# Optimization experiments

Hardware: AMD Instinct MI355X
Metric: run time of the kernel (lower is better)

The kernel has to match this reference:

```python
import jax, jax.numpy as jnp
import numpy as np

H, N, L = 1024, 64, 2          # d_model, d_state, n_layers
B, T, STEPS = 32, 512, 16


def setup_inputs():
    key = jax.random.key(0)
    ks = jax.random.split(key, 12)
    inp = {}
    inp["input_seq"] = jax.random.normal(ks[0], (B, T, 1), jnp.float32)
    inp["autoregressive_steps"] = STEPS
    # input_proj: Linear(1, d_model)
    inp["in_proj_w"] = jax.random.normal(ks[1], (1, H), jnp.float32)
    inp["in_proj_b"] = jnp.zeros((H,), jnp.float32)
    # per-layer diagonal S4 (S4D-style) params, stacked over layers
    inp["log_dt"] = jnp.log(1e-3) + jax.random.uniform(ks[2], (L, H), jnp.float32) * (jnp.log(1e-1) - jnp.log(1e-3))
    inp["A_re"] = -0.5 * jnp.ones((L, H, N), jnp.float32)
    inp["A_im"] = jnp.broadcast_to(jnp.pi * jnp.arange(N, dtype=jnp.float32), (L, H, N)) + jnp.zeros((L, H, N), jnp.float32)
    inp["B_re"] = jax.random.normal(ks[3], (L, H, N), jnp.float32)
    inp["B_im"] = jax.random.normal(ks[4], (L, H, N), jnp.float32)
    inp["C_re"] = jax.random.normal(ks[5], (L, H, N), jnp.float32) / np.sqrt(N)
    inp["C_im"] = jax.random.normal(ks[6], (L, H, N), jnp.float32) / np.sqrt(N)
    inp["D"] = jax.random.normal(ks[7], (L, H), jnp.float32)
    # S4Block output linear with GLU: Linear(H, 2H) then glu
    inp["out_w"] = jax.random.normal(ks[8], (L, H, 2 * H), jnp.float32) / np.sqrt(H)
    inp["out_b"] = jnp.zeros((L, 2 * H), jnp.float32)
    inp["ln_g"] = jnp.ones((L, H), jnp.float32)
    inp["ln_b"] = jnp.zeros((L, H), jnp.float32)
    # output_layer: Linear(d_model, 1)
    inp["head_w"] = jax.random.normal(ks[9], (H, 1), jnp.float32) / np.sqrt(H)
    inp["head_b"] = jnp.zeros((1,), jnp.float32)
    return inp


def _ln(x, g, b, eps=1e-5):
    m = x.mean(-1, keepdims=True)
    v = jnp.var(x, axis=-1, keepdims=True)
    return (x - m) / jnp.sqrt(v + eps) * g + b


def _glu(z):
    a, b = jnp.split(z, 2, axis=-1)
    return a * jax.nn.sigmoid(b)


def _forward(input_seq, in_proj_w, in_proj_b, log_dt, A_re, A_im, B_re, B_im,
             C_re, C_im, D, out_w, out_b, ln_g, ln_b, head_w, head_b, steps):
    Bb = input_seq.shape[0]
    A = A_re + 1j * A_im                              # (L,H,N) complex64
    dt = jnp.exp(log_dt)[..., None]                   # (L,H,1)
    dA = jnp.exp(dt * A)                              # ZOH discretization
    dB = (dA - 1.0) / A * (B_re + 1j * B_im)
    C = C_re + 1j * C_im

    def s4_seq(u, j):  # u: (B,T,H) -> (B,T,H), recurrence over the full sequence
        s0 = jnp.zeros((Bb, H, N), dA.dtype)
        def step(s, ut):  # ut: (B,H)
            s = dA[j] * s + dB[j] * ut[..., None]
            y = 2.0 * jnp.einsum('hn,bhn->bh', C[j], s).real + D[j] * ut
            return s, y
        _, ys = jax.lax.scan(step, s0, jnp.swapaxes(u, 0, 1))
        return jnp.swapaxes(ys, 0, 1)

    # ---- encoder pass over the input sequence ----
    x = input_seq @ in_proj_w + in_proj_b             # (B,T,H)
    for j in range(L):
        res = x
        y = s4_seq(x, j)
        y = jax.nn.gelu(y, approximate=False)
        y = _glu(y @ out_w[j] + out_b[j])
        x = _ln(y + res, ln_g[j], ln_b[j])
    context = x[:, -1, :]                             # (B,H)

    def dec_step(carry, i):
        dec_in, states = carry                        # (B,), (L,B,H,N) complex
        u0 = jnp.broadcast_to(dec_in[:, None], (Bb, H))   # scalar broadcast to d_model
        dec = u0
        new_states = []
        for j in range(L):
            s = dA[j] * states[j] + dB[j] * dec[..., None]
            y = 2.0 * jnp.einsum('hn,bhn->bh', C[j], s).real + D[j] * dec
            y = jax.nn.gelu(y, approximate=False)
            y = _glu(y @ out_w[j] + out_b[j])
            res = jnp.where(i == 0, u0, y)            # step 0: raw-input residual; else self-residual
            dec = _ln(y + res, ln_g[j], ln_b[j])
            new_states.append(s)
        dec = dec + context
        bit = jax.nn.sigmoid(dec @ head_w + head_b)   # (B,1)
        return (bit[:, 0], jnp.stack(new_states)), bit

    s_init = jnp.zeros((L, Bb, H, N), dA.dtype)
    d_init = jnp.zeros((Bb,), input_seq.dtype)
    _, outs = jax.lax.scan(dec_step, (d_init, s_init), jnp.arange(steps))
    return jnp.swapaxes(outs, 0, 1)                   # (B, steps, 1)


def reference(input_seq, in_proj_w, in_proj_b, log_dt, A_re, A_im, B_re, B_im,
              C_re, C_im, D, out_w, out_b, ln_g, ln_b, head_w, head_b,
              autoregressive_steps):
    return _forward(input_seq, in_proj_w, in_proj_b, log_dt, A_re, A_im, B_re,
                    B_im, C_re, C_im, D, out_w, out_b, ln_g, ln_b, head_w,
                    head_b, autoregressive_steps)
```

## Files before the change

### kernel.cpp

```cpp
#include <hip/hip_runtime.h>
#include <hip/hip_bf16.h>
#include <math.h>

#define H    1024
#define NST  64
#define LAYN 2
#define BSZ  32
#define TLEN 512
#define NSTEPS 16
#define H2   2048
#define FLAGSTRIDE 32
#define NGRP 8

typedef __attribute__((ext_vector_type(8))) short bf16x8;
typedef __attribute__((ext_vector_type(4))) float f32x4;

__device__ __forceinline__ float gelu_f(float x){
    return 0.5f*x*(1.0f+erff(x*0.7071067811865475f));
}
__device__ __forceinline__ float sigm_f(float x){
    return 1.0f/(1.0f+expf(-x));
}
__device__ __forceinline__ short bfbits(float x){
    __hip_bfloat16 h = __float2bfloat16(x);
    return *(short*)&h;
}
__device__ __forceinline__ float bf2f(short s){
    unsigned int u = ((unsigned int)(unsigned short)s) << 16;
    return __uint_as_float(u);
}
__device__ __forceinline__ void gload16(const void* g, void* l){
    __builtin_amdgcn_global_load_lds((const __attribute__((address_space(1))) void*)g,
                                     (__attribute__((address_space(3))) void*)l, 16, 0, 0);
}
__device__ __forceinline__ void ast(float* p, float v){
    __hip_atomic_store(p, v, __ATOMIC_RELAXED, __HIP_MEMORY_SCOPE_AGENT);
}
__device__ __forceinline__ float ald(const float* p){
    return __hip_atomic_load(p, __ATOMIC_RELAXED, __HIP_MEMORY_SCOPE_AGENT);
}

__global__ void k_precompute(const float* __restrict__ log_dt,
                             const float* __restrict__ Are, const float* __restrict__ Aim,
                             const float* __restrict__ Bre, const float* __restrict__ Bim,
                             float* __restrict__ dAr, float* __restrict__ dAi,
                             float* __restrict__ dBr, float* __restrict__ dBi){
    int i = blockIdx.x*256 + threadIdx.x;
    if (i >= LAYN*H*NST) return;
    int lh = i / NST;
    float dt = expf(log_dt[lh]);
    float ar = Are[i], ai = Aim[i];
    float e  = expf(dt*ar);
    float sa, ca; sincosf(dt*ai, &sa, &ca);
    float dar = e*ca, dai = e*sa;
    float zr = dar-1.0f, zi = dai;
    float inv = 1.0f/(ar*ar + ai*ai);
    float wr = (zr*ar + zi*ai)*inv;
    float wi = (zi*ar - zr*ai)*inv;
    float br = Bre[i], bi = Bim[i];
    dAr[i]=dar; dAi[i]=dai;
    dBr[i]=wr*br - wi*bi;
    dBi[i]=wr*bi + wi*br;
}

__global__ void k_inproj_x(const float* __restrict__ in, const float* __restrict__ w,
                           const float* __restrict__ bias, float* __restrict__ x){
    int i = blockIdx.x*256+threadIdx.x;
    int h = i & (H-1);
    int bt = i >> 10;
    x[i] = in[bt]*w[h] + bias[h];
}
__global__ void k_inproj_xT(const float* __restrict__ in, const float* __restrict__ w,
                            const float* __restrict__ bias, float* __restrict__ xT){
    int i = blockIdx.x*256+threadIdx.x;
    int t = i & (TLEN-1);
    int bh = i >> 9;
    int h = bh & (H-1);
    int b = bh >> 10;
    xT[i] = in[b*TLEN + t]*w[h] + bias[h];
}

__global__ __launch_bounds__(64) void k_genK(
        const float* __restrict__ dAr, const float* __restrict__ dAi,
        const float* __restrict__ dBr, const float* __restrict__ dBi,
        const float* __restrict__ Cre, const float* __restrict__ Cim,
        float* __restrict__ Kbuf){
    __shared__ float trans[16][65];
    int lh = blockIdx.x;
    int lane = threadIdx.x;
    int pi = lh*NST + lane;
    float ar=dAr[pi], ai=dAi[pi];
    float br=dBr[pi], bi=dBi[pi];
    float cr=2.f*Cre[pi], ci=2.f*Cim[pi];
    float wr = cr*br - ci*bi;
    float wi = cr*bi + ci*br;
    float* Krow = Kbuf + (size_t)lh*TLEN;
    int r = lane>>2, q = lane&3;
    for (int c=0;c<TLEN/16;c++){
        #pragma unroll
        for (int i=0;i<16;i++){
            trans[i][lane] = wr;
            float nr = fmaf(wr,ar, -wi*ai);
            float ni = fmaf(wr,ai,  wi*ar);
            wr=nr; wi=ni;
        }
        __syncthreads();
        float s = 0.f;
        #pragma unroll
        for (int m=0;m<16;m++) s += trans[r][q*16+m];
        s += __shfl_xor(s,1,64);
        s += __shfl_xor(s,2,64);
        if (q==0) Krow[c*16 + r] = s;
        __syncthreads();
    }
}

__global__ __launch_bounds__(256, 2) void k_conv_mfma(
        const float* __restrict__ u,
        const float* __restrict__ Kbuf,
        const float* __restrict__ Dv,
        __hip_bfloat16* __restrict__ g,
        int layer){
    __shared__ short Krp[8][1040];
    __shared__ short u_s[32][520];
    int h = blockIdx.x;
    int tid = threadIdx.x;
    const float* Krow = Kbuf + ((size_t)layer*H + h)*TLEN;
    for (int idx = tid; idx < 8*1040; idx += 256){
        int c = idx / 1040, y = idx - c*1040;
        int x = y + c;
        float v = (x <= 511) ? Krow[511 - x] : 0.f;
        Krp[c][y] = bfbits(v);
    }
    for (int idx = tid; idx < 32*512; idx += 256){
        int b = idx >> 9, t = idx & 511;
        u_s[b][t] = bfbits(u[((size_t)b*H + h)*TLEN + t]);
    }
    __syncthreads();
    int w = tid >> 6, lane = tid & 63;
    int m = lane & 15, q = lane >> 4;
    f32x4 acc[8][2] = {};
    for (int jt = 0; jt < 16; ++jt){
        int jtile = jt*32;
        bf16x8 b0 = *(const bf16x8*)&u_s[m][jtile + q*8];
        bf16x8 b1 = *(const bf16x8*)&u_s[16 + m][jtile + q*8];
        int mi_min = (2*jt - w + 3) >> 2;
        if (mi_min < 0) mi_min = 0;
        #pragma unroll
        for (int mi = 0; mi < 8; ++mi){
            if (mi < mi_min) continue;
            int tb = (mi*4 + w)*16 + m;
            int x0 = 511 - tb + jtile + q*8;
            int c = x0 & 7, base = x0 - c;
            bf16x8 a = *(const bf16x8*)&Krp[c][base];
            acc[mi][0] = __builtin_amdgcn_mfma_f32_16x16x32_bf16(a, b0, acc[mi][0], 0,0,0);
            acc[mi][1] = __builtin_amdgcn_mfma_f32_16x16x32_bf16(a, b1, acc[mi][1], 0,0,0);
        }
    }
    float dv = Dv[layer*H + h];
    #pragma unroll
    for (int mi = 0; mi < 8; ++mi){
        int tb2 = (mi*4 + w)*16 + (lane>>4)*4;
        #pragma unroll
        for (int nf = 0; nf < 2; ++nf){
            int b = nf*16 + (lane & 15);
            short4 o;
            float uu0 = bf2f(u_s[b][tb2+0]);
            float uu1 = bf2f(u_s[b][tb2+1]);
            float uu2 = bf2f(u_s[b][tb2+2]);
            float uu3 = bf2f(u_s[b][tb2+3]);
            o.x = bfbits(gelu_f(fmaf(dv, uu0, acc[mi][nf][0])));
            o.y = bfbits(gelu_f(fmaf(dv, uu1, acc[mi][nf][1])));
            o.z = bfbits(gelu_f(fmaf(dv, uu2, acc[mi][nf][2])));
            o.w = bfbits(gelu_f(fmaf(dv, uu3, acc[mi][nf][3])));
            *(short4*)((short*)g + ((size_t)b*H + h)*TLEN + tb2) = o;
        }
    }
}

__global__ __launch_bounds__(256) void k_trcast_bf(const __hip_bfloat16* __restrict__ x,
                                                   __hip_bfloat16* __restrict__ y){
    __shared__ __hip_bfloat16 tile[32][34];
    int t0 = blockIdx.x*32, h0 = blockIdx.y*32, b = blockIdx.z;
    int tx = threadIdx.x & 31, ty = threadIdx.x >> 5;
    #pragma unroll
    for (int i=0;i<32;i+=8)
        tile[ty+i][tx] = x[((size_t)(b*H + h0+ty+i))*TLEN + t0+tx];
    __syncthreads();
    #pragma unroll
    for (int i=0;i<32;i+=8)
        y[((size_t)(b*TLEN + t0+ty+i))*H + h0+tx] = tile[tx][ty+i];
}

__global__ __launch_bounds__(256) void k_transpose(const float* __restrict__ x, float* __restrict__ xT){
    __shared__ float tile[32][33];
    int t0 = blockIdx.x*32, h0 = blockIdx.y*32, b = blockIdx.z;
    int tx = threadIdx.x & 31, ty = threadIdx.x >> 5;
    #pragma unroll
    for (int i=0;i<32;i+=8)
        tile[ty+i][tx] = x[((size_t)(b*TLEN + t0+ty+i))*H + h0+tx];
    __syncthreads();
    #pragma unroll
    for (int i=0;i<32;i+=8)
        xT[((size_t)(b*H + h0+ty+i))*TLEN + t0+tx] = tile[tx][ty+i];
}

__global__ __launch_bounds__(256) void k_wtr(const float* __restrict__ W,
                                             __hip_bfloat16* __restrict__ Wt){
    __shared__ float tile[32][33];
    int n0 = blockIdx.x*32, k0 = blockIdx.y*32, l = blockIdx.z;
    const float* Wl = W + (size_t)l*H*H2;
    __hip_bfloat16* Wtl = Wt + (size_t)l*H*H2;
    int tx = threadIdx.x & 31, ty = threadIdx.x >> 5;
    #pragma unroll
    for (int i=0;i<32;i+=8)
        tile[ty+i][tx] = Wl[(size_t)(k0+ty+i)*H2 + n0+tx];
    __syncthreads();
    #pragma unroll
    for (int i=0;i<32;i+=8)
        Wtl[(size_t)(n0+ty+i)*H + k0+tx] = __float2bfloat16(tile[tx][ty+i]);
}

__global__ __launch_bounds__(256) void k_gemm_glu_mfma(
        const __hip_bfloat16* __restrict__ Abf,
        const __hip_bfloat16* __restrict__ Wt,
        const float* __restrict__ bias2,
        float* __restrict__ glu){
    __shared__ alignas(16) short As[128*32];
    __shared__ alignas(16) short Bs[128*32];
    const int K = 1024;
    int tid = threadIdx.x;
    int lane = tid & 63, wid = tid >> 6;
    int m0 = blockIdx.x * 128;
    int nb = blockIdx.y * 64;
    int g0 = tid, g1 = tid + 256;
    int r0 = g0 >> 2, r1 = g1 >> 2;
    int wtr0 = nb + ((r0>>6)<<5) + (r0&31) + ((r0>>5)&1)*1024;
    int wtr1 = nb + ((r1>>6)<<5) + (r1&31) + ((r1>>5)&1)*1024;
    const short* Ap = (const short*)Abf;
    const short* Bp = (const short*)Wt;
    const short* Ag0 = Ap + (size_t)(m0 + r0)*K + (g0&3)*8;
    const short* Ag1 = Ap + (size_t)(m0 + r1)*K + (g1&3)*8;
    const short* Bg0 = Bp + (size_t)wtr0*K + (g0&3)*8;
    const short* Bg1 = Bp + (size_t)wtr1*K + (g1&3)*8;
    char* AsB = (char*)As;
    char* BsB = (char*)Bs;
    int wr = wid >> 1, wc = wid & 1;
    int mo = wr*64, no = wc*64;
    f32x4 acc[4][4] = {};
    int arow = (lane & 15)*32 + (lane>>4)*8;
    for (int k0 = 0; k0 < K; k0 += 32){
        gload16(Ag0 + k0, AsB + wid*1024);
        gload16(Ag1 + k0, AsB + 4096 + wid*1024);
        gload16(Bg0 + k0, BsB + wid*1024);
        gload16(Bg1 + k0, BsB + 4096 + wid*1024);
        asm volatile("s_waitcnt vmcnt(0)" ::: "memory");
        __syncthreads();
        bf16x8 a[4], b[4];
        #pragma unroll
        for (int mi=0;mi<4;mi++)
            a[mi] = *(const bf16x8*)(As + (mo + mi*16)*32 + arow);
        #pragma unroll
        for (int ni=0;ni<4;ni++)
            b[ni] = *(const bf16x8*)(Bs + (no + ni*16)*32 + arow);
        #pragma unroll
        for (int mi=0;mi<4;mi++){
            #pragma unroll
            for (int ni=0;ni<4;ni++){
                acc[mi][ni] = __builtin_amdgcn_mfma_f32_16x16x32_bf16(a[mi], b[ni], acc[mi][ni], 0, 0, 0);
            }
        }
        __syncthreads();
    }
    int cbase = nb + wc*32 + (lane&15);
    #pragma unroll
    for (int ni=0;ni<2;ni++){
        int c = cbase + ni*16;
        float ba = bias2[c], bb = bias2[c+1024];
        #pragma unroll
        for (int mi=0;mi<4;mi++){
            #pragma unroll
            for (int r=0;r<4;r++){
                size_t m = m0 + mo + mi*16 + (lane>>4)*4 + r;
                float za = acc[mi][ni][r] + ba;
                float zb = acc[mi][ni+2][r] + bb;
                glu[m*H + c] = za * sigm_f(zb);
            }
        }
    }
}

__global__ __launch_bounds__(256) void k_ln(const float* __restrict__ glu, const float* __restrict__ res,
        const float* __restrict__ gamma, const float* __restrict__ beta, float* __restrict__ outx){
    __shared__ float red[8];
    int row = blockIdx.x;
    int tid = threadIdx.x;
    float4 gv = *(const float4*)(glu + (size_t)row*H + tid*4);
    float4 rv = *(const float4*)(res + (size_t)row*H + tid*4);
    float x0=gv.x+rv.x, x1=gv.y+rv.y, x2=gv.z+rv.z, x3=gv.w+rv.w;
    float s = x0+x1+x2+x3;
    float q = x0*x0+x1*x1+x2*x2+x3*x3;
    #pragma unroll
    for (int m=32;m>=1;m>>=1){ s += __shfl_xor(s,m,64); q += __shfl_xor(q,m,64); }
    int wv = tid>>6;
    if ((tid&63)==0){ red[wv]=s; red[4+wv]=q; }
    __syncthreads();
    s = red[0]+red[1]+red[2]+red[3];
    q = red[4]+red[5]+red[6]+red[7];
    float m = s*(1.0f/H);
    float v = q*(1.0f/H) - m*m;
    float rstd = rsqrtf(v + 1e-5f);
    float4 gm = *(const float4*)(gamma + tid*4);
    float4 bt = *(const float4*)(beta + tid*4);
    float4 o;
    o.x = (x0-m)*rstd*gm.x + bt.x;
    o.y = (x1-m)*rstd*gm.y + bt.y;
    o.z = (x2-m)*rstd*gm.z + bt.z;
    o.w = (x3-m)*rstd*gm.w + bt.w;
    *(float4*)(outx + (size_t)row*H + tid*4) = o;
}

__global__ void k_ctx(const float* __restrict__ x, float* __restrict__ ctx){
    int i = blockIdx.x*256+threadIdx.x;
    int b = i>>10, h = i&(H-1);
    ctx[i] = x[((size_t)(b*TLEN + TLEN-1))*H + h];
}

__device__ __forceinline__ void gbar_grp(int* gfl, int jj, int g, int tid){
    __syncthreads();
    if (tid == 0)
        __hip_atomic_store(gfl + jj*FLAGSTRIDE, g, __ATOMIC_RELAXED,
                           __HIP_MEMORY_SCOPE_AGENT);
    if (tid < 32){
        int it = 0;
        while (__hip_atomic_load(gfl + tid*FLAGSTRIDE, __ATOMIC_RELAXED,
                                 __HIP_MEMORY_SCOPE_AGENT) < g){
            __builtin_amdgcn_s_sleep(1);
            if (++it > 1000000) break;
        }
    }
    __syncthreads();
}

__device__ __forceinline__ void gemv4(int grp, int jj, int tid,
        float (*ysh)[H], float (*part)[32][8],
        const short* __restrict__ Wl, const float* __restrict__ b2,
        const float* __restrict__ ygel, float* __restrict__ glud){
    #pragma unroll
    for (int i=0;i<16;i++){
        int idx = i*256 + tid;
        int b4 = idx >> 10, hh = idx & 1023;
        ysh[b4][hh] = ald(&ygel[(size_t)(4*grp + b4)*H + hh]);
    }
    __syncthreads();
    int p = tid & 31, ks = tid >> 5;
    int colp = jj*32 + p;
    const short* wza = Wl + (size_t)colp*H + ks*128;
    const short* wzb = Wl + (size_t)(colp+1024)*H + ks*128;
    float a0=0,a1=0,a2=0,a3=0, c0=0,c1=0,c2=0,c3=0;
    const float* u0 = &ysh[0][ks*128];
    const float* u1 = &ysh[1][ks*128];
    const float* u2 = &ysh[2][ks*128];
    const float* u3 = &ysh[3][ks*128];
    for (int kk=0; kk<128; kk+=8){
        bf16x8 wa = *(const bf16x8*)(wza + kk);
        bf16x8 wb = *(const bf16x8*)(wzb + kk);
        #pragma unroll
        for (int j=0;j<8;j++){
            float wav = bf2f(wa[j]), wbv = bf2f(wb[j]);
            float y0 = u0[kk+j], y1 = u1[kk+j], y2 = u2[kk+j], y3 = u3[kk+j];
            a0 = fmaf(y0, wav, a0);  c0 = fmaf(y0, wbv, c0);
            a1 = fmaf(y1, wav, a1);  c1 = fmaf(y1, wbv, c1);
            a2 = fmaf(y2, wav, a2);  c2 = fmaf(y2, wbv, c2);
            a3 = fmaf(y3, wav, a3);  c3 = fmaf(y3, wbv, c3);
        }
    }
    __syncthreads();
    part[ks][p][0]=a0; part[ks][p][1]=c0;
    part[ks][p][2]=a1; part[ks][p][3]=c1;
    part[ks][p][4]=a2; part[ks][p][5]=c2;
    part[ks][p][6]=a3; part[ks][p][7]=c3;
    __syncthreads();
    if (tid < 128){
        int p2 = tid & 31, b4 = tid >> 5;
        int c2 = jj*32 + p2;
        float sa=0.f, sb=0.f;
        #pragma unroll
        for (int q=0;q<8;q++){ sa += part[q][p2][b4*2]; sb += part[q][p2][b4*2+1]; }
        float za = sa + b2[c2];
        float zb = sb + b2[1024 + c2];
        ast(&glud[(size_t)(4*grp + b4)*H + c2], za * sigm_f(zb));
    }
}

__global__ __launch_bounds__(256, 1) void k_decode(
        const float* __restrict__ Kbuf, const float* __restrict__ Dv,
        const __hip_bfloat16* __restrict__ Wt, const float* __restrict__ bias2,
        const float* __restrict__ lng, const float* __restrict__ lnb,
        const float* __restrict__ ctx, const float* __restrict__ headw,
        const float* __restrict__ headb,
        float* __restrict__ ygel0, float* __restrict__ ygel1,
        float* __restrict__ glud0, float* __restrict__ glud1,
        float* __restrict__ out, int* __restrict__ flags){
    __shared__ float hist[16][H];
    __shared__ float ysh[4][H];
    __shared__ float part[8][32][8];
    __shared__ float red[8];
    __shared__ float bitsh[16];
    int bid = blockIdx.x;
    int grp = bid & 7, jj = bid >> 3;
    int tid = threadIdx.x;
    int lane = tid & 63, wv = tid >> 6;
    bool leader = (jj < 4);
    int b = grp*4 + jj;
    float4 dv0v, dv1v, lg0v, be0v, lg1v, be1v, cvxv, hwv;
    float hb = headb[0];
    if (leader){
        dv0v = *(const float4*)(Dv + tid*4);
        dv1v = *(const float4*)(Dv + H + tid*4);
        lg0v = *(const float4*)(lng + tid*4);
        be0v = *(const float4*)(lnb + tid*4);
        lg1v = *(const float4*)(lng + H + tid*4);
        be1v = *(const float4*)(lnb + H + tid*4);
        cvxv = *(const float4*)(ctx + (size_t)b*H + tid*4);
        hwv  = *(const float4*)(headw + tid*4);
    }
    if (tid < 16) bitsh[tid] = 0.f;
    __syncthreads();
    const short* Wt0 = (const short*)Wt;
    const short* Wt1 = (const short*)Wt + (size_t)H*H2;
    int* gfl = flags + grp*32*FLAGSTRIDE;
    int g = 1;
    for (int s=0; s<NSTEPS; s++){
        if (leader){
            if (s > 0){
                int sp = s-1;
                float x0 = ald(&glud1[(size_t)b*H + tid*4+0]);
                float x1 = ald(&glud1[(size_t)b*H + tid*4+1]);
                float x2 = ald(&glud1[(size_t)b*H + tid*4+2]);
                float x3 = ald(&glud1[(size_t)b*H + tid*4+3]);
                if (sp != 0){ x0*=2.f; x1*=2.f; x2*=2.f; x3*=2.f; }
                float su = x0+x1+x2+x3, qu = x0*x0+x1*x1+x2*x2+x3*x3;
                #pragma unroll
                for (int m=32;m>=1;m>>=1){ su += __shfl_xor(su,m,64); qu += __shfl_xor(qu,m,64); }
                if (lane==0){ red[wv]=su; red[4+wv]=qu; }
                __syncthreads();
                float S = red[0]+red[1]+red[2]+red[3];
                float Q = red[4]+red[5]+red[6]+red[7];
                float mean = S*(1.f/H), var = Q*(1.f/H)-mean*mean;
                float rstd = rsqrtf(var + 1e-5f);
                float d0 = (x0-mean)*rstd*lg1v.x + be1v.x + cvxv.x;
                float d1 = (x1-mean)*rstd*lg1v.y + be1v.y + cvxv.y;
                float d2 = (x2-mean)*rstd*lg1v.z + be1v.z + cvxv.z;
                float d3 = (x3-mean)*rstd*lg1v.w + be1v.w + cvxv.w;
                float hp = d0*hwv.x + d1*hwv.y + d2*hwv.z + d3*hwv.w;
                #pragma unroll
                for (int m=32;m>=1;m>>=1) hp += __shfl_xor(hp,m,64);
                __syncthreads();
                if (lane==0) red[wv] = hp;
                __syncthreads();
                float hs = red[0]+red[1]+red[2]+red[3] + hb;
                float bit = sigm_f(hs);
                if (tid==0){ out[b*NSTEPS + sp] = bit; bitsh[sp] = bit; }
                __syncthreads();
            }
            float bu = (s==0) ? 0.f : bitsh[s-1];
            float dvs[4] = {dv0v.x, dv0v.y, dv0v.z, dv0v.w};
            #pragma unroll
            for (int i=0;i<4;i++){
                int h = tid*4+i;
                const float* Kr = Kbuf + (size_t)h*TLEN;
                float y0 = dvs[i]*bu;
                #pragma unroll
                for (int d=0; d<16; d++){
                    int idx = s-1-d;
                    float uv = (idx >= 0) ? bitsh[idx] : 0.f;
                    y0 = fmaf(Kr[d], uv, y0);
                }
                ast(&ygel0[(size_t)b*H + h], gelu_f(y0));
            }
        }
        gbar_grp(gfl, jj, g++, tid);
        gemv4(grp, jj, tid, ysh, part, Wt0, bias2, ygel0, glud0);
        gbar_grp(gfl, jj, g++, tid);
        if (leader){
            float x0 = ald(&glud0[(size_t)b*H + tid*4+0]);
            float x1 = ald(&glud0[(size_t)b*H + tid*4+1]);
            float x2 = ald(&glud0[(size_t)b*H + tid*4+2]);
            float x3 = ald(&glud0[(size_t)b*H + tid*4+3]);
            if (s != 0){ x0*=2.f; x1*=2.f; x2*=2.f; x3*=2.f; }
            float su = x0+x1+x2+x3, qu = x0*x0+x1*x1+x2*x2+x3*x3;
            #pragma unroll
            for (int m=32;m>=1;m>>=1){ su += __shfl_xor(su,m,64); qu += __shfl_xor(qu,m,64); }
            if (lane==0){ red[wv]=su; red[4+wv]=qu; }
            __syncthreads();
            float S = red[0]+red[1]+red[2]+red[3];
            float Q = red[4]+red[5]+red[6]+red[7];
            float mean = S*(1.f/H), var = Q*(1.f/H)-mean*mean;
            float rstd = rsqrtf(var + 1e-5f);
            float dd[4];
            dd[0] = (x0-mean)*rstd*lg0v.x + be0v.x;
            dd[1] = (x1-mean)*rstd*lg0v.y + be0v.y;
            dd[2] = (x2-mean)*rstd*lg0v.z + be0v.z;
            dd[3] = (x3-mean)*rstd*lg0v.w + be0v.w;
            float dvs[4] = {dv1v.x, dv1v.y, dv1v.z, dv1v.w};
            #pragma unroll
            for (int i=0;i<4;i++){
                int h = tid*4+i;
                hist[s & 15][h] = dd[i];
                const float* Kr = Kbuf + (size_t)(H+h)*TLEN;
                float y1 = dvs[i]*dd[i];
                #pragma unroll
                for (int d=0; d<16; d++){
                    int sd = s-d;
                    float uv = (sd >= 0) ? hist[sd & 15][h] : 0.f;
                    y1 = fmaf(Kr[d], uv, y1);
                }
                ast(&ygel1[(size_t)b*H + h], gelu_f(y1));
            }
        }
        gbar_grp(gfl, jj, g++, tid);
        gemv4(grp, jj, tid, ysh, part, Wt1, bias2 + H2, ygel1, glud1);
        gbar_grp(gfl, jj, g++, tid);
    }
    if (leader){
        float x0 = 2.f*ald(&glud1[(size_t)b*H + tid*4+0]);
        float x1 = 2.f*ald(&glud1[(size_t)b*H + tid*4+1]);
        float x2 = 2.f*ald(&glud1[(size_t)b*H + tid*4+2]);
        float x3 = 2.f*ald(&glud1[(size_t)b*H + tid*4+3]);
        float su = x0+x1+x2+x3, qu = x0*x0+x1*x1+x2*x2+x3*x3;
        #pragma unroll
        for (int m=32;m>=1;m>>=1){ su += __shfl_xor(su,m,64); qu += __shfl_xor(qu,m,64); }
        if (lane==0){ red[wv]=su; red[4+wv]=qu; }
        __syncthreads();
        float S = red[0]+red[1]+red[2]+red[3];
        float Q = red[4]+red[5]+red[6]+red[7];
        float mean = S*(1.f/H), var = Q*(1.f/H)-mean*mean;
        float rstd = rsqrtf(var + 1e-5f);
        float d0 = (x0-mean)*rstd*lg1v.x + be1v.x + cvxv.x;
        float d1 = (x1-mean)*rstd*lg1v.y + be1v.y + cvxv.y;
        float d2 = (x2-mean)*rstd*lg1v.z + be1v.z + cvxv.z;
        float d3 = (x3-mean)*rstd*lg1v.w + be1v.w + cvxv.w;
        float hp = d0*hwv.x + d1*hwv.y + d2*hwv.z + d3*hwv.w;
        #pragma unroll
        for (int m=32;m>=1;m>>=1) hp += __shfl_xor(hp,m,64);
        __syncthreads();
        if (lane==0) red[wv] = hp;
        __syncthreads();
        float hs = red[0]+red[1]+red[2]+red[3] + hb;
        if (tid==0) out[b*NSTEPS + 15] = sigm_f(hs);
    }
}

extern "C" void kernel_launch(void* const* d_in, const int* in_sizes, int n_in,
                              void* d_out, int out_size, void* d_ws, size_t ws_size,
                              hipStream_t stream) {
    const float* in_seq = (const float*)d_in[0];
    const float* inw  = (const float*)d_in[2];
    const float* inb  = (const float*)d_in[3];
    const float* log_dt = (const float*)d_in[4];
    const float* Are = (const float*)d_in[5];
    const float* Aim = (const float*)d_in[6];
    const float* Bre = (const float*)d_in[7];
    const float* Bim = (const float*)d_in[8];
    const float* Cre = (const float*)d_in[9];
    const float* Cim = (const float*)d_in[10];
    const float* Dv  = (const float*)d_in[11];
    const float* outw = (const float*)d_in[12];
    const float* outb = (const float*)d_in[13];
    const float* lng = (const float*)d_in[14];
    const float* lnb = (const float*)d_in[15];
    const float* headw = (const float*)d_in[16];
    const float* headb = (const float*)d_in[17];
    float* out = (float*)d_out;

    float* ws = (float*)d_ws;
    size_t off = 0;
    auto alloc = [&](size_t n){ float* p = ws + off; off += n; return p; };
    float* dAr = alloc((size_t)LAYN*H*NST);
    float* dAi = alloc((size_t)LAYN*H*NST);
    float* dBr = alloc((size_t)LAYN*H*NST);
    float* dBi = alloc((size_t)LAYN*H*NST);
    float* Kbuf = alloc((size_t)LAYN*H*TLEN);
    float* bufA = alloc((size_t)BSZ*TLEN*H);
    float* bufB = alloc((size_t)BSZ*TLEN*H);
    __hip_bfloat16* gbf = (__hip_bfloat16*)alloc((size_t)BSZ*TLEN*H/2);
    __hip_bfloat16* Abf = (__hip_bfloat16*)alloc((size_t)BSZ*TLEN*H/2);
    __hip_bfloat16* Wt  = (__hip_bfloat16*)alloc((size_t)LAYN*H*H2/2);
    float* ctx = alloc((size_t)BSZ*H);
    float* ygel0 = alloc((size_t)BSZ*H);
    float* ygel1 = alloc((size_t)BSZ*H);
    float* glud0 = alloc((size_t)BSZ*H);
    float* glud1 = alloc((size_t)BSZ*H);
    int*   flags = (int*)alloc((size_t)NGRP*32*FLAGSTRIDE);

    k_precompute<<<(LAYN*H*NST+255)/256, 256, 0, stream>>>(log_dt,Are,Aim,Bre,Bim,dAr,dAi,dBr,dBi);
    k_genK<<<LAYN*H, 64, 0, stream>>>(dAr,dAi,dBr,dBi,Cre,Cim,Kbuf);
    k_wtr<<<dim3(H2/32, H/32, LAYN), 256, 0, stream>>>(outw, Wt);
    k_inproj_x <<<(BSZ*TLEN*H)/256, 256, 0, stream>>>(in_seq, inw, inb, bufA);
    k_inproj_xT<<<(BSZ*TLEN*H)/256, 256, 0, stream>>>(in_seq, inw, inb, bufB);

    k_conv_mfma<<<dim3(H), 256, 0, stream>>>(bufB, Kbuf, Dv, gbf, 0);
    k_trcast_bf<<<dim3(TLEN/32, H/32, BSZ), 256, 0, stream>>>(gbf, Abf);
    k_gemm_glu_mfma<<<dim3(BSZ*TLEN/128, H/64), 256, 0, stream>>>(Abf, Wt, outb, bufB);
    k_ln<<<BSZ*TLEN, 256, 0, stream>>>(bufB, bufA, lng, lnb, bufA);
    k_transpose<<<dim3(16,32,32), 256, 0, stream>>>(bufA, bufB);

    k_conv_mfma<<<dim3(H), 256, 0, stream>>>(bufB, Kbuf, Dv, gbf, 1);
    k_trcast_bf<<<dim3(TLEN/32, H/32, BSZ), 256, 0, stream>>>(gbf, Abf);
    k_gemm_glu_mfma<<<dim3(BSZ*TLEN/128, H/64), 256, 0, stream>>>(Abf, Wt + (size_t)H*H2, outb + H2, bufB);
    k_ln<<<BSZ*TLEN, 256, 0, stream>>>(bufB, bufA, lng+H, lnb+H, bufA);

    k_ctx<<<(BSZ*H)/256, 256, 0, stream>>>(bufA, ctx);

    hipMemsetAsync(flags, 0, sizeof(int)*(size_t)NGRP*32*FLAGSTRIDE, stream);
    k_decode<<<NGRP*32, 256, 0, stream>>>(Kbuf, Dv, Wt, outb, lng, lnb,
                                          ctx, headw, headb,
                                          ygel0, ygel1, glud0, glud1, out, flags);
}
```

Baseline: 1.237 ms.

## Restructure decode GEMV to per-column slices over all batches with global hierarchical barrier

The decode kernel previously split the 256 blocks into 8 independent groups of 4 batch rows, so each group re-read the whole output weight matrix. Now each block computes 4 output columns (plus their gate columns) for all 32 batch rows, so each weight column is read once per step across the grid. Because every block now needs every batch row's activations, synchronisation becomes a two-level grid-wide barrier (per-XCD, then across XCDs) instead of per-group barriers. Activations and the conv history are stored as bf16 to shrink the exchanged data and LDS, which adds rounding error.

Result: slower. 1.606 ms (+29.9%).

```diff
diff --git a/kernel.cpp b/kernel.cpp
--- a/kernel.cpp
+++ b/kernel.cpp
@@ -10,9 +10,9 @@
 #define NSTEPS 16
 #define H2   2048
 #define FLAGSTRIDE 32
-#define NGRP 8
 
 typedef __attribute__((ext_vector_type(8))) short bf16x8;
+typedef __attribute__((ext_vector_type(4))) short bf16x4;
 typedef __attribute__((ext_vector_type(4))) float f32x4;
 
 __device__ __forceinline__ float gelu_f(float x){
@@ -37,6 +37,12 @@
     __hip_atomic_store(p, v, __ATOMIC_RELAXED, __HIP_MEMORY_SCOPE_AGENT);
 }
 __device__ __forceinline__ float ald(const float* p){
+    return __hip_atomic_load(p, __ATOMIC_RELAXED, __HIP_MEMORY_SCOPE_AGENT);
+}
+__device__ __forceinline__ void astu(unsigned int* p, unsigned int v){
+    __hip_atomic_store(p, v, __ATOMIC_RELAXED, __HIP_MEMORY_SCOPE_AGENT);
+}
+__device__ __forceinline__ unsigned int aldu(const unsigned int* p){
     return __hip_atomic_load(p, __ATOMIC_RELAXED, __HIP_MEMORY_SCOPE_AGENT);
 }
 
@@ -326,14 +332,40 @@
     ctx[i] = x[((size_t)(b*TLEN + TLEN-1))*H + h];
 }
 
-__device__ __forceinline__ void gbar_grp(int* gfl, int jj, int g, int tid){
+__device__ __forceinline__ void hbar(int* bar, int xcd, int j, int g, int tid){
     __syncthreads();
     if (tid == 0)
-        __hip_atomic_store(gfl + jj*FLAGSTRIDE, g, __ATOMIC_RELAXED,
+        __hip_atomic_store(&bar[(xcd*32 + j)*FLAGSTRIDE], g, __ATOMIC_RELAXED,
                            __HIP_MEMORY_SCOPE_AGENT);
-    if (tid < 32){
+    if (j == 0){
+        if (tid < 32){
+            int it = 0;
+            while (__hip_atomic_load(&bar[(xcd*32 + tid)*FLAGSTRIDE], __ATOMIC_RELAXED,
+                                     __HIP_MEMORY_SCOPE_AGENT) < g){
+                __builtin_amdgcn_s_sleep(1);
+                if (++it > 1000000) break;
+            }
+        }
+        __syncthreads();
+        if (tid == 0)
+            __hip_atomic_store(&bar[(256 + xcd)*FLAGSTRIDE], g, __ATOMIC_RELAXED,
+                               __HIP_MEMORY_SCOPE_AGENT);
+        if (tid < 8){
+            int it = 0;
+            while (__hip_atomic_load(&bar[(256 + tid)*FLAGSTRIDE], __ATOMIC_RELAXED,
+                                     __HIP_MEMORY_SCOPE_AGENT) < g){
+                __builtin_amdgcn_s_sleep(1);
+                if (++it > 1000000) break;
+            }
+        }
+        __syncthreads();
+        if (tid == 0)
+            __hip_atomic_store(&bar[(264 + xcd)*FLAGSTRIDE], g, __ATOMIC_RELAXED,
+                               __HIP_MEMORY_SCOPE_AGENT);
+    }
+    if (tid == 0){
         int it = 0;
-        while (__hip_atomic_load(gfl + tid*FLAGSTRIDE, __ATOMIC_RELAXED,
+        while (__hip_atomic_load(&bar[(264 + xcd)*FLAGSTRIDE], __ATOMIC_RELAXED,
                                  __HIP_MEMORY_SCOPE_AGENT) < g){
             __builtin_amdgcn_s_sleep(1);
             if (++it > 1000000) break;
@@ -342,54 +374,61 @@
     __syncthreads();
 }
 
-__device__ __forceinline__ void gemv4(int grp, int jj, int tid,
-        float (*ysh)[H], float (*part)[32][8],
+__device__ __forceinline__ void gemm_slice(int cp0, int tid,
+        unsigned short (*u_s)[1028], float (*part)[4][2][32],
         const short* __restrict__ Wl, const float* __restrict__ b2,
-        const float* __restrict__ ygel, float* __restrict__ glud){
-    #pragma unroll
-    for (int i=0;i<16;i++){
+        const unsigned int* __restrict__ ygel, float* __restrict__ glud){
+    #pragma unroll 4
+    for (int i = 0; i < 64; ++i){
         int idx = i*256 + tid;
-        int b4 = idx >> 10, hh = idx & 1023;
-        ysh[b4][hh] = ald(&ygel[(size_t)(4*grp + b4)*H + hh]);
-    }
-    __syncthreads();
-    int p = tid & 31, ks = tid >> 5;
-    int colp = jj*32 + p;
-    const short* wza = Wl + (size_t)colp*H + ks*128;
-    const short* wzb = Wl + (size_t)(colp+1024)*H + ks*128;
-    float a0=0,a1=0,a2=0,a3=0, c0=0,c1=0,c2=0,c3=0;
-    const float* u0 = &ysh[0][ks*128];
-    const float* u1 = &ysh[1][ks*128];
-    const float* u2 = &ysh[2][ks*128];
-    const float* u3 = &ysh[3][ks*128];
-    for (int kk=0; kk<128; kk+=8){
-        bf16x8 wa = *(const bf16x8*)(wza + kk);
-        bf16x8 wb = *(const bf16x8*)(wzb + kk);
-        #pragma unroll
-        for (int j=0;j<8;j++){
-            float wav = bf2f(wa[j]), wbv = bf2f(wb[j]);
-            float y0 = u0[kk+j], y1 = u1[kk+j], y2 = u2[kk+j], y3 = u3[kk+j];
-            a0 = fmaf(y0, wav, a0);  c0 = fmaf(y0, wbv, c0);
-            a1 = fmaf(y1, wav, a1);  c1 = fmaf(y1, wbv, c1);
-            a2 = fmaf(y2, wav, a2);  c2 = fmaf(y2, wbv, c2);
-            a3 = fmaf(y3, wav, a3);  c3 = fmaf(y3, wbv, c3);
-        }
-    }
-    __syncthreads();
-    part[ks][p][0]=a0; part[ks][p][1]=c0;
-    part[ks][p][2]=a1; part[ks][p][3]=c1;
-    part[ks][p][4]=a2; part[ks][p][5]=c2;
-    part[ks][p][6]=a3; part[ks][p][7]=c3;
+        int bb = idx >> 9, k2 = idx & 511;
+        unsigned int v = aldu(&ygel[bb*512 + k2]);
+        *(unsigned int*)&u_s[bb][k2*2] = v;
+    }
+    __syncthreads();
+    int b = tid & 31, ks = tid >> 5;
+    const unsigned short* ub = &u_s[b][ks*128];
+    float accA[4], accB[4];
+    #pragma unroll
+    for (int c = 0; c < 4; ++c){
+        const short* wa = Wl + (size_t)(cp0 + c)*H + ks*128;
+        const short* wb = Wl + (size_t)(cp0 + c + 1024)*H + ks*128;
+        float aa = 0.f, ab = 0.f;
+        #pragma unroll 4
+        for (int kk = 0; kk < 128; kk += 8){
+            bf16x8 wva = *(const bf16x8*)(wa + kk);
+            bf16x8 wvb = *(const bf16x8*)(wb + kk);
+            bf16x4 u0 = *(const bf16x4*)(ub + kk);
+            bf16x4 u1 = *(const bf16x4*)(ub + kk + 4);
+            #pragma unroll
+            for (int q = 0; q < 4; ++q){
+                float uv = bf2f(u0[q]);
+                aa = fmaf(uv, bf2f(wva[q]), aa);
+                ab = fmaf(uv, bf2f(wvb[q]), ab);
+            }
+            #pragma unroll
+            for (int q = 0; q < 4; ++q){
+                float uv = bf2f(u1[q]);
+                aa = fmaf(uv, bf2f(wva[4+q]), aa);
+                ab = fmaf(uv, bf2f(wvb[4+q]), ab);
+            }
+        }
+        accA[c] = aa; accB[c] = ab;
+    }
+    __syncthreads();
+    #pragma unroll
+    for (int c = 0; c < 4; ++c){
+        part[ks][c][0][b] = accA[c];
+        part[ks][c][1][b] = accB[c];
+    }
     __syncthreads();
     if (tid < 128){
-        int p2 = tid & 31, b4 = tid >> 5;
-        int c2 = jj*32 + p2;
-        float sa=0.f, sb=0.f;
-        #pragma unroll
-        for (int q=0;q<8;q++){ sa += part[q][p2][b4*2]; sb += part[q][p2][b4*2+1]; }
-        float za = sa + b2[c2];
-        float zb = sb + b2[1024 + c2];
-        ast(&glud[(size_t)(4*grp + b4)*H + c2], za * sigm_f(zb));
+        int bb = tid & 31, c = tid >> 5;
+        float sa = 0.f, sb = 0.f;
+        #pragma unroll
+        for (int q = 0; q < 8; ++q){ sa += part[q][c][0][bb]; sb += part[q][c][1][bb]; }
+        int col = cp0 + c;
+        ast(&glud[(size_t)bb*H + col], (sa + b2[col]) * sigm_f(sb + b2[1024 + col]));
     }
 }
 
@@ -399,20 +438,21 @@
         const float* __restrict__ lng, const float* __restrict__ lnb,
         const float* __restrict__ ctx, const float* __restrict__ headw,
         const float* __restrict__ headb,
-        float* __restrict__ ygel0, float* __restrict__ ygel1,
+        unsigned int* __restrict__ ygel0, unsigned int* __restrict__ ygel1,
         float* __restrict__ glud0, float* __restrict__ glud1,
-        float* __restrict__ out, int* __restrict__ flags){
-    __shared__ float hist[16][H];
-    __shared__ float ysh[4][H];
-    __shared__ float part[8][32][8];
+        float* __restrict__ out, int* __restrict__ bar){
+    __shared__ unsigned short u_s[32][1028];
+    __shared__ unsigned short hist[16][1024];
+    __shared__ float part[8][4][2][32];
     __shared__ float red[8];
     __shared__ float bitsh[16];
     int bid = blockIdx.x;
-    int grp = bid & 7, jj = bid >> 3;
+    int xcd = bid & 7, j = bid >> 3;
     int tid = threadIdx.x;
     int lane = tid & 63, wv = tid >> 6;
-    bool leader = (jj < 4);
-    int b = grp*4 + jj;
+    bool leader = (j < 4);
+    int b = j*8 + xcd;
+    int cp0 = xcd*128 + j*4;
     float4 dv0v, dv1v, lg0v, be0v, lg1v, be1v, cvxv, hwv;
     float hb = headb[0];
     if (leader){
@@ -429,9 +469,8 @@
     __syncthreads();
     const short* Wt0 = (const short*)Wt;
     const short* Wt1 = (const short*)Wt + (size_t)H*H2;
-    int* gfl = flags + grp*32*FLAGSTRIDE;
     int g = 1;
-    for (int s=0; s<NSTEPS; s++){
+    for (int s = 0; s < NSTEPS; ++s){
         if (leader){
             if (s > 0){
                 int sp = s-1;
@@ -466,6 +505,7 @@
             }
             float bu = (s==0) ? 0.f : bitsh[s-1];
             float dvs[4] = {dv0v.x, dv0v.y, dv0v.z, dv0v.w};
+            float yv[4];
             #pragma unroll
             for (int i=0;i<4;i++){
                 int h = tid*4+i;
@@ -477,12 +517,18 @@
                     float uv = (idx >= 0) ? bitsh[idx] : 0.f;
                     y0 = fmaf(Kr[d], uv, y0);
                 }
-                ast(&ygel0[(size_t)b*H + h], gelu_f(y0));
-            }
-        }
-        gbar_grp(gfl, jj, g++, tid);
-        gemv4(grp, jj, tid, ysh, part, Wt0, bias2, ygel0, glud0);
-        gbar_grp(gfl, jj, g++, tid);
+                yv[i] = gelu_f(y0);
+            }
+            unsigned int p0 = (unsigned int)(unsigned short)bfbits(yv[0]) |
+                              ((unsigned int)(unsigned short)bfbits(yv[1]) << 16);
+            unsigned int p1 = (unsigned int)(unsigned short)bfbits(yv[2]) |
+                              ((unsigned int)(unsigned short)bfbits(yv[3]) << 16);
+            astu(&ygel0[b*512 + tid*2],     p0);
+            astu(&ygel0[b*512 + tid*2 + 1], p1);
+        }
+        hbar(bar, xcd, j, g++, tid);
+        gemm_slice(cp0, tid, u_s, part, Wt0, bias2, ygel0, glud0);
+        hbar(bar, xcd, j, g++, tid);
         if (leader){
             float x0 = ald(&glud0[(size_t)b*H + tid*4+0]);
             float x1 = ald(&glud0[(size_t)b*H + tid*4+1]);
@@ -504,24 +550,31 @@
             dd[2] = (x2-mean)*rstd*lg0v.z + be0v.z;
             dd[3] = (x3-mean)*rstd*lg0v.w + be0v.w;
             float dvs[4] = {dv1v.x, dv1v.y, dv1v.z, dv1v.w};
+            float yv[4];
             #pragma unroll
             for (int i=0;i<4;i++){
                 int h = tid*4+i;
-                hist[s & 15][h] = dd[i];
+                hist[s & 15][h] = (unsigned short)bfbits(dd[i]);
                 const float* Kr = Kbuf + (size_t)(H+h)*TLEN;
                 float y1 = dvs[i]*dd[i];
                 #pragma unroll
                 for (int d=0; d<16; d++){
                     int sd = s-d;
-                    float uv = (sd >= 0) ? hist[sd & 15][h] : 0.f;
+                    float uv = (sd >= 0) ? bf2f((short)hist[sd & 15][h]) : 0.f;
                     y1 = fmaf(Kr[d], uv, y1);
                 }
-                ast(&ygel1[(size_t)b*H + h], gelu_f(y1));
-            }
-        }
-        gbar_grp(gfl, jj, g++, tid);
-        gemv4(grp, jj, tid, ysh, part, Wt1, bias2 + H2, ygel1, glud1);
-        gbar_grp(gfl, jj, g++, tid);
+                yv[i] = gelu_f(y1);
+            }
+            unsigned int p0 = (unsigned int)(unsigned short)bfbits(yv[0]) |
+                              ((unsigned int)(unsigned short)bfbits(yv[1]) << 16);
+            unsigned int p1 = (unsigned int)(unsigned short)bfbits(yv[2]) |
+                              ((unsigned int)(unsigned short)bfbits(yv[3]) << 16);
+            astu(&ygel1[b*512 + tid*2],     p0);
+            astu(&ygel1[b*512 + tid*2 + 1], p1);
+        }
+        hbar(bar, xcd, j, g++, tid);
+        gemm_slice(cp0, tid, u_s, part, Wt1, bias2 + H2, ygel1, glud1);
+        hbar(bar, xcd, j, g++, tid);
     }
     if (leader){
         float x0 = 2.f*ald(&glud1[(size_t)b*H + tid*4+0]);
@@ -588,11 +641,11 @@
     __hip_bfloat16* Abf = (__hip_bfloat16*)alloc((size_t)BSZ*TLEN*H/2);
     __hip_bfloat16* Wt  = (__hip_bfloat16*)alloc((size_t)LAYN*H*H2/2);
     float* ctx = alloc((size_t)BSZ*H);
-    float* ygel0 = alloc((size_t)BSZ*H);
-    float* ygel1 = alloc((size_t)BSZ*H);
+    unsigned int* ygel0 = (unsigned int*)alloc((size_t)BSZ*512);
+    unsigned int* ygel1 = (unsigned int*)alloc((size_t)BSZ*512);
     float* glud0 = alloc((size_t)BSZ*H);
     float* glud1 = alloc((size_t)BSZ*H);
-    int*   flags = (int*)alloc((size_t)NGRP*32*FLAGSTRIDE);
+    int*   bar  = (int*)alloc((size_t)272*FLAGSTRIDE);
 
     k_precompute<<<(LAYN*H*NST+255)/256, 256, 0, stream>>>(log_dt,Are,Aim,Bre,Bim,dAr,dAi,dBr,dBi);
     k_genK<<<LAYN*H, 64, 0, stream>>>(dAr,dAi,dBr,dBi,Cre,Cim,Kbuf);
@@ -613,8 +666,8 @@
 
     k_ctx<<<(BSZ*H)/256, 256, 0, stream>>>(bufA, ctx);
 
-    hipMemsetAsync(flags, 0, sizeof(int)*(size_t)NGRP*32*FLAGSTRIDE, stream);
-    k_decode<<<NGRP*32, 256, 0, stream>>>(Kbuf, Dv, Wt, outb, lng, lnb,
-                                          ctx, headw, headb,
-                                          ygel0, ygel1, glud0, glud1, out, flags);
-}
+    hipMemsetAsync(bar, 0, sizeof(int)*(size_t)272*FLAGSTRIDE, stream);
+    k_decode<<<256, 256, 0, stream>>>(Kbuf, Dv, Wt, outb, lng, lnb,
+                                      ctx, headw, headb,
+                                      ygel0, ygel1, glud0, glud1, out, bar);
+}
```
